# Performance work log

Hardware: AMD Instinct MI355X
Metric: run time of the kernel (lower is better)

The kernel has to match this reference:

```python
import jax, jax.numpy as jnp
import numpy as np

B, T, D, H, L = 32, 512, 1024, 1024, 2


def setup_inputs() -> dict:
    key = jax.random.key(0)
    ks = jax.random.split(key, 7)
    s_in = 1.0 / np.sqrt(D)
    s_h = 1.0 / np.sqrt(H)
    return {
        "x": jax.random.normal(ks[0], (B, T, D), dtype=jnp.float32),
        # layer 0: input_size = D
        "W_ih0": jax.random.uniform(ks[1], (4 * H, D), jnp.float32, -s_in, s_in),
        "b0": jax.random.uniform(ks[2], (4 * H,), jnp.float32, -s_in, s_in),
        "W_hh0": jax.random.uniform(ks[3], (4 * H, H), jnp.float32, -s_h, s_h),
        # layer 1: input_size = H
        "W_ih1": jax.random.uniform(ks[4], (4 * H, H), jnp.float32, -s_h, s_h),
        "b1": jax.random.uniform(ks[5], (4 * H,), jnp.float32, -s_h, s_h),
        "W_hh1": jax.random.uniform(ks[6], (4 * H, H), jnp.float32, -s_h, s_h),
    }


def _lstm_layer(x_seq, W_ih, b, W_hh):
    # x_seq: [T, B, Din]. Precompute the input-to-gate GEMM for all steps
    # (mathematically identical to per-step, but one big GEMM).
    gx = jnp.einsum('tbd,gd->tbg', x_seq, W_ih) + b  # [T, B, 4H]
    h0 = jnp.zeros((x_seq.shape[1], W_hh.shape[1]), x_seq.dtype)
    c0 = jnp.zeros_like(h0)

    def step(carry, gx_t):
        h, c = carry
        gates = gx_t + h @ W_hh.T  # [B, 4H]
        i, f, g, o = jnp.split(gates, 4, axis=-1)  # torch chunk order: i,f,g,o
        i = jax.nn.sigmoid(i)
        f = jax.nn.sigmoid(f)
        g = jnp.tanh(g)
        o = jax.nn.sigmoid(o)
        c_new = f * c + i * g
        h_new = o * jnp.tanh(c_new)
        return (h_new, c_new), h_new

    (h_n, c_n), hs = jax.lax.scan(step, (h0, c0), gx)
    return hs, h_n, c_n  # hs: [T, B, H]


def reference(x, W_ih0, b0, W_hh0, W_ih1, b1, W_hh1):
    xs = jnp.transpose(x, (1, 0, 2))  # batch_first -> [T, B, D]
    hs0, h0_n, c0_n = _lstm_layer(xs, W_ih0, b0, W_hh0)
    hs1, h1_n, c1_n = _lstm_layer(hs0, W_ih1, b1, W_hh1)
    output = jnp.transpose(hs1, (1, 0, 2))  # [B, T, H]
    h_n = jnp.stack([h0_n, h1_n], axis=0)  # [L, B, H]
    c_n = jnp.stack([c0_n, c1_n], axis=0)
    return output, (h_n, c_n)
```

## Files before the change

### kernel.cpp

```cpp
#include <hip/hip_runtime.h>
#include <stdint.h>

typedef __attribute__((ext_vector_type(8))) short short8;
typedef __attribute__((ext_vector_type(4))) short short4v;
typedef __attribute__((ext_vector_type(4))) float f32x4;
typedef __attribute__((ext_vector_type(4))) unsigned int u32x4;
typedef __attribute__((ext_vector_type(4))) int i32x4;
typedef __attribute__((ext_vector_type(2))) unsigned long long u64x2;

__device__ inline unsigned short f2bf(float f) {
  unsigned int u = __builtin_bit_cast(unsigned int, f);
  u += 0x7fffu + ((u >> 16) & 1u);
  return (unsigned short)(u >> 16);
}
__device__ inline float bf2f(unsigned short s) {
  return __builtin_bit_cast(float, (unsigned int)s << 16);
}

__device__ inline unsigned long long stale64(unsigned long long v) {
  unsigned long long x = v ^ 0x7f7f7f7f7f7f7f7full;
  return (x - 0x0001000100010001ull) & ~x & 0x8000800080008000ull;
}


__global__ __launch_bounds__(256) void cvt_x_kernel(const float* __restrict__ x,
                                                    short* __restrict__ xbf) {
  const int total = (16384 * 1024) / 4;
  for (int i = blockIdx.x * blockDim.x + threadIdx.x; i < total;
       i += gridDim.x * blockDim.x) {
    int d4 = i & 255;
    int m  = i >> 8;
    int t = m >> 5, b = m & 31;
    float4 v = *(const float4*)(x + ((size_t)b * 512 + t) * 1024 + (size_t)d4 * 4);
    short4v o;
    o.x = (short)f2bf(v.x); o.y = (short)f2bf(v.y);
    o.z = (short)f2bf(v.z); o.w = (short)f2bf(v.w);
    *(short4v*)(xbf + (size_t)m * 1024 + d4 * 4) = o;
  }
}

__global__ __launch_bounds__(256) void cvt_w_kernel(const float* __restrict__ W,
                                                    short* __restrict__ Wp) {
  const int total = (4096 * 1024) / 4;
  for (int i = blockIdx.x * blockDim.x + threadIdx.x; i < total;
       i += gridDim.x * blockDim.x) {
    int k4 = i & 255;
    int n  = i >> 8;
    int g = n & 3, j = n >> 2;
    float4 v = *(const float4*)(W + ((size_t)g * 1024 + j) * 1024 + (size_t)k4 * 4);
    short4v o;
    o.x = (short)f2bf(v.x); o.y = (short)f2bf(v.y);
    o.z = (short)f2bf(v.z); o.w = (short)f2bf(v.w);
    *(short4v*)(Wp + (size_t)n * 1024 + k4 * 4) = o;
  }
}

__global__ __launch_bounds__(256) void cvt_b_kernel(const float* __restrict__ b,
                                                    float* __restrict__ bp) {
  int n = blockIdx.x * blockDim.x + threadIdx.x;
  if (n < 4096) bp[n] = b[(n & 3) * 1024 + (n >> 2)];
}

__global__ __launch_bounds__(256) void gemm_bt(const short* __restrict__ A,
                                               const short* __restrict__ Bm,
                                               short* __restrict__ C) {
  const int n0 = blockIdx.x * 128;
  const int m0 = blockIdx.y * 128;
  const int tid = threadIdx.x;
  const int lane = tid & 63, wid = tid >> 6;
  const int wr = wid >> 1, wc = wid & 1;
  const int fr = lane & 15, fq = lane >> 4;

  __shared__ __align__(16) short As[128 * 32];
  __shared__ __align__(16) short Bs[128 * 32];

  f32x4 acc[4][4];
#pragma unroll
  for (int i = 0; i < 4; i++)
#pragma unroll
    for (int j = 0; j < 4; j++) acc[i][j] = (f32x4){0.f, 0.f, 0.f, 0.f};

  for (int kt = 0; kt < 1024; kt += 32) {
#pragma unroll
    for (int s = 0; s < 2; s++) {
      int c = tid + s * 256;
      int row = c >> 2;
      int off = (c & 3) * 8;
      *(u32x4*)&As[row * 32 + off] =
          *(const u32x4*)(A + (size_t)(n0 + row) * 1024 + kt + off);
      *(u32x4*)&Bs[row * 32 + off] =
          *(const u32x4*)(Bm + (size_t)(m0 + row) * 1024 + kt + off);
    }
    __syncthreads();
    short8 af[4], bf[4];
#pragma unroll
    for (int i = 0; i < 4; i++)
      af[i] = *(const short8*)&As[(wr * 64 + i * 16 + fr) * 32 + fq * 8];
#pragma unroll
    for (int j = 0; j < 4; j++)
      bf[j] = *(const short8*)&Bs[(wc * 64 + j * 16 + fr) * 32 + fq * 8];
#pragma unroll
    for (int i = 0; i < 4; i++)
#pragma unroll
      for (int j = 0; j < 4; j++)
        acc[i][j] = __builtin_amdgcn_mfma_f32_16x16x32_bf16(af[i], bf[j], acc[i][j], 0, 0, 0);
    __syncthreads();
  }

#pragma unroll
  for (int i = 0; i < 4; i++) {
#pragma unroll
    for (int j = 0; j < 4; j++) {
      int nq = n0 + wr * 64 + i * 16 + fq * 4;
      int m = m0 + wc * 64 + j * 16 + fr;
      int t = m >> 5, b = m & 31;
      unsigned long long pk = 0;
#pragma unroll
      for (int r = 0; r < 4; r++)
        pk |= (unsigned long long)f2bf(acc[i][j][r]) << (16 * r);
      *(unsigned long long*)&C[(size_t)t * 131072 + (size_t)b * 4096 + nq] = pk;
    }
  }
}

#define POLL8(HBP)                                                            \
  do {                                                                        \
    i32x4 r0, r1, r2, r3, r4, r5, r6, r7;                                     \
    while (true) {                                                            \
      asm volatile(                                                           \
          "global_load_dwordx4 %0, %8, %16 sc0 sc1\n\t"                       \
          "global_load_dwordx4 %1, %9, %16 sc0 sc1\n\t"                       \
          "global_load_dwordx4 %2, %10, %16 sc0 sc1\n\t"                      \
          "global_load_dwordx4 %3, %11, %16 sc0 sc1\n\t"                      \
          "global_load_dwordx4 %4, %12, %16 sc0 sc1\n\t"                      \
          "global_load_dwordx4 %5, %13, %16 sc0 sc1\n\t"                      \
          "global_load_dwordx4 %6, %14, %16 sc0 sc1\n\t"                      \
          "global_load_dwordx4 %7, %15, %16 sc0 sc1\n\t"                      \
          "s_waitcnt vmcnt(0)"                                                \
          : "=&v"(r0), "=&v"(r1), "=&v"(r2), "=&v"(r3), "=&v"(r4),            \
            "=&v"(r5), "=&v"(r6), "=&v"(r7)                                   \
          : "v"(soff[0]), "v"(soff[1]), "v"(soff[2]), "v"(soff[3]),           \
            "v"(soff[4]), "v"(soff[5]), "v"(soff[6]), "v"(soff[7]),           \
            "s"(HBP)                                                          \
          : "memory");                                                        \
      u64x2 q0 = __builtin_bit_cast(u64x2, r0), q1 = __builtin_bit_cast(u64x2, r1); \
      u64x2 q2 = __builtin_bit_cast(u64x2, r2), q3 = __builtin_bit_cast(u64x2, r3); \
      u64x2 q4 = __builtin_bit_cast(u64x2, r4), q5 = __builtin_bit_cast(u64x2, r5); \
      u64x2 q6 = __builtin_bit_cast(u64x2, r6), q7 = __builtin_bit_cast(u64x2, r7); \
      unsigned long long bad =                                                \
          stale64(q0.x) | stale64(q0.y) | stale64(q1.x) | stale64(q1.y) |     \
          stale64(q2.x) | stale64(q2.y) | stale64(q3.x) | stale64(q3.y) |     \
          stale64(q4.x) | stale64(q4.y) | stale64(q5.x) | stale64(q5.y) |     \
          stale64(q6.x) | stale64(q6.y) | stale64(q7.x) | stale64(q7.y);      \
      if (!bad) break;                                                        \
    }                                                                         \
    *(i32x4*)&img[widx[0]] = r0;                                              \
    *(i32x4*)&img[widx[1]] = r1;                                              \
    *(i32x4*)&img[widx[2]] = r2;                                              \
    *(i32x4*)&img[widx[3]] = r3;                                              \
    *(i32x4*)&img[widx[4]] = r4;                                              \
    *(i32x4*)&img[widx[5]] = r5;                                              \
    *(i32x4*)&img[widx[6]] = r6;                                              \
    *(i32x4*)&img[widx[7]] = r7;                                              \
  } while (0)

__global__ __launch_bounds__(512, 1) void lstm_fused(
    const short* __restrict__ gx0, const short* __restrict__ whh0,
    const float* __restrict__ b0p, const short* __restrict__ wih1,
    const short* __restrict__ whh1, const float* __restrict__ b1p,
    short* __restrict__ hs0, short* __restrict__ hs1,
    float* __restrict__ out, float* __restrict__ hn, float* __restrict__ cn) {
  const int tid = threadIdx.x;
  const int lane = tid & 63, w = tid >> 6;
  const int fr = lane & 15, fq = lane >> 4;

  __shared__ __align__(16) short img[32 * 1024];
  __shared__ __align__(16) float red[4 * 64 * 4];

  if (blockIdx.x < 64) {
    const int rg = (int)blockIdx.x >> 1, bg = (int)blockIdx.x & 1;
    const int n_base = rg * 128 + w * 16;
    const int b = bg * 16 + fr;
    const int jb = rg * 32 + w * 4;
    const int j = jb + fq;
    const int sw = fr & 7;

    const short* arow = whh0 + (size_t)(n_base + fr) * 1024 + fq * 8;
    short8 wreg[32];
#pragma unroll
    for (int kk = 0; kk < 32; kk++) wreg[kk] = *(const short8*)(arow + kk * 32);

    float bia[4];
#pragma unroll
    for (int r = 0; r < 4; r++) bia[r] = b0p[n_base + fq * 4 + r];

    unsigned int soff[4];
    int widx[4];
#pragma unroll
    for (int i = 0; i < 4; i++) {
      int ch = tid + i * 512;
      soff[i] = (unsigned int)ch * 16;
      int bb = ch >> 7, cc = ch & 127;
      widx[i] = bb * 1024 + ((cc ^ (bb & 7)) << 3);
    }

    float cell = 0.f;
    for (int t = 0; t < 512; ++t) {
      unsigned long long gq = *(const unsigned long long*)(
          gx0 + (size_t)t * 131072 + (size_t)b * 4096 + n_base + fq * 4);

      if (t > 0) {
        const short* hbp = hs0 + (size_t)(t - 1) * 32768 + bg * 16384;
        i32x4 r0, r1, r2, r3;
        while (true) {
          asm volatile(
              "global_load_dwordx4 %0, %4, %8 sc0 sc1\n\t"
              "global_load_dwordx4 %1, %5, %8 sc0 sc1\n\t"
              "global_load_dwordx4 %2, %6, %8 sc0 sc1\n\t"
              "global_load_dwordx4 %3, %7, %8 sc0 sc1\n\t"
              "s_waitcnt vmcnt(0)"
              : "=&v"(r0), "=&v"(r1), "=&v"(r2), "=&v"(r3)
              : "v"(soff[0]), "v"(soff[1]), "v"(soff[2]), "v"(soff[3]),
                "s"(hbp)
              : "memory");
          u64x2 q0 = __builtin_bit_cast(u64x2, r0);
          u64x2 q1 = __builtin_bit_cast(u64x2, r1);
          u64x2 q2 = __builtin_bit_cast(u64x2, r2);
          u64x2 q3 = __builtin_bit_cast(u64x2, r3);
          unsigned long long bad =
              stale64(q0.x) | stale64(q0.y) | stale64(q1.x) | stale64(q1.y) |
              stale64(q2.x) | stale64(q2.y) | stale64(q3.x) | stale64(q3.y);
          if (!bad) break;
        }
        *(i32x4*)&img[widx[0]] = r0;
        *(i32x4*)&img[widx[1]] = r1;
        *(i32x4*)&img[widx[2]] = r2;
        *(i32x4*)&img[widx[3]] = r3;
      }
      __syncthreads();

      f32x4 a0 = (f32x4){0.f,0.f,0.f,0.f}, a1 = (f32x4){0.f,0.f,0.f,0.f};
      f32x4 a2 = (f32x4){0.f,0.f,0.f,0.f}, a3 = (f32x4){0.f,0.f,0.f,0.f};
      if (t > 0) {
#pragma unroll
        for (int m = 0; m < 8; m++) {
          const int chb = fq + m * 16;
          short8 bv0 = *(const short8*)&img[fr * 1024 + (((chb + 0) ^ sw) << 3)];
          short8 bv1 = *(const short8*)&img[fr * 1024 + (((chb + 4) ^ sw) << 3)];
          short8 bv2 = *(const short8*)&img[fr * 1024 + (((chb + 8) ^ sw) << 3)];
          short8 bv3 = *(const short8*)&img[fr * 1024 + (((chb + 12) ^ sw) << 3)];
          a0 = __builtin_amdgcn_mfma_f32_16x16x32_bf16(wreg[4 * m + 0], bv0, a0, 0, 0, 0);
          a1 = __builtin_amdgcn_mfma_f32_16x16x32_bf16(wreg[4 * m + 1], bv1, a1, 0, 0, 0);
          a2 = __builtin_amdgcn_mfma_f32_16x16x32_bf16(wreg[4 * m + 2], bv2, a2, 0, 0, 0);
          a3 = __builtin_amdgcn_mfma_f32_16x16x32_bf16(wreg[4 * m + 3], bv3, a3, 0, 0, 0);
        }
      }

      float pre0 = (a0[0] + a1[0]) + (a2[0] + a3[0]) + bf2f((unsigned short)(gq & 0xFFFF)) + bia[0];
      float pre1 = (a0[1] + a1[1]) + (a2[1] + a3[1]) + bf2f((unsigned short)((gq >> 16) & 0xFFFF)) + bia[1];
      float pre2 = (a0[2] + a1[2]) + (a2[2] + a3[2]) + bf2f((unsigned short)((gq >> 32) & 0xFFFF)) + bia[2];
      float pre3 = (a0[3] + a1[3]) + (a2[3] + a3[3]) + bf2f((unsigned short)((gq >> 48) & 0xFFFF)) + bia[3];

      float iv = 1.f / (1.f + __expf(-pre0));
      float fv = 1.f / (1.f + __expf(-pre1));
      float gv = 2.f / (1.f + __expf(-2.f * pre2)) - 1.f;
      float ov = 1.f / (1.f + __expf(-pre3));
      cell = fv * cell + iv * gv;
      float h = ov * (2.f / (1.f + __expf(-2.f * cell)) - 1.f);

      unsigned int hu = (unsigned int)f2bf(h);
      unsigned int v1 = __shfl(hu, fr + 16);
      unsigned int v2 = __shfl(hu, fr + 32);
      unsigned int v3 = __shfl(hu, fr + 48);
      if (fq == 0) {
        unsigned long long pk = (unsigned long long)hu |
                                ((unsigned long long)v1 << 16) |
                                ((unsigned long long)v2 << 32) |
                                ((unsigned long long)v3 << 48);
        __hip_atomic_store(
            (unsigned long long*)(hs0 + (size_t)t * 32768 + (size_t)b * 1024 + jb),
            pk, __ATOMIC_RELAXED, __HIP_MEMORY_SCOPE_AGENT);
      }
      if (t == 511) {
        hn[b * 1024 + j] = h;
        cn[b * 1024 + j] = cell;
        break;
      }
      __syncthreads();
    }
  } else {
    const int idx = (int)blockIdx.x - 64;
    const int rg = idx >> 1, bg = idx & 1;
    const int wn = w & 3, mw = w >> 2;
    const int n_base = rg * 64 + wn * 16;
    const int b = bg * 16 + fr;
    const int jb = rg * 16 + wn * 4;
    const int j = jb + fq;
    const int sw = fr & 7;
    const int ib = mw << 14;

    const short* wsrc = mw ? wih1 : whh1;
    const short* arow = wsrc + (size_t)(n_base + fr) * 1024 + fq * 8;
    short8 wreg[32];
#pragma unroll
    for (int kk = 0; kk < 32; kk++) wreg[kk] = *(const short8*)(arow + kk * 32);

    float bia[4];
#pragma unroll
    for (int r = 0; r < 4; r++) bia[r] = b1p[n_base + fq * 4 + r];

    const int lt = tid & 255;
    unsigned int soff[8];
    int widx[8];
#pragma unroll
    for (int i = 0; i < 8; i++) {
      int ch = lt + i * 256;
      soff[i] = (unsigned int)ch * 16;
      int bb = ch >> 7, cc = ch & 127;
      widx[i] = ib + bb * 1024 + ((cc ^ (bb & 7)) << 3);
    }

    float cell = 0.f;
    for (int t = 0; t < 512; ++t) {
      if (mw) {
        const short* hbp = hs0 + (size_t)t * 32768 + bg * 16384;
        POLL8(hbp);
      } else if (t > 0) {
        const short* hbp = hs1 + (size_t)(t - 1) * 32768 + bg * 16384;
        POLL8(hbp);
      }
      __syncthreads();

      f32x4 a0 = (f32x4){0.f,0.f,0.f,0.f}, a1 = (f32x4){0.f,0.f,0.f,0.f};
      f32x4 a2 = (f32x4){0.f,0.f,0.f,0.f}, a3 = (f32x4){0.f,0.f,0.f,0.f};
      if (mw || t > 0) {
#pragma unroll
        for (int m = 0; m < 8; m++) {
          const int chb = fq + m * 16;
          short8 bv0 = *(const short8*)&img[ib + fr * 1024 + (((chb + 0) ^ sw) << 3)];
          short8 bv1 = *(const short8*)&img[ib + fr * 1024 + (((chb + 4) ^ sw) << 3)];
          short8 bv2 = *(const short8*)&img[ib + fr * 1024 + (((chb + 8) ^ sw) << 3)];
          short8 bv3 = *(const short8*)&img[ib + fr * 1024 + (((chb + 12) ^ sw) << 3)];
          a0 = __builtin_amdgcn_mfma_f32_16x16x32_bf16(wreg[4 * m + 0], bv0, a0, 0, 0, 0);
          a1 = __builtin_amdgcn_mfma_f32_16x16x32_bf16(wreg[4 * m + 1], bv1, a1, 0, 0, 0);
          a2 = __builtin_amdgcn_mfma_f32_16x16x32_bf16(wreg[4 * m + 2], bv2, a2, 0, 0, 0);
          a3 = __builtin_amdgcn_mfma_f32_16x16x32_bf16(wreg[4 * m + 3], bv3, a3, 0, 0, 0);
        }
      }
      f32x4 s4 = (a0 + a1) + (a2 + a3);
      if (mw) *(f32x4*)&red[(wn * 64 + lane) * 4] = s4;
      __syncthreads();

      if (!mw) {
        const f32x4 o4 = *(const f32x4*)&red[(wn * 64 + lane) * 4];
        float pre0 = s4[0] + o4[0] + bia[0];
        float pre1 = s4[1] + o4[1] + bia[1];
        float pre2 = s4[2] + o4[2] + bia[2];
        float pre3 = s4[3] + o4[3] + bia[3];

        float iv = 1.f / (1.f + __expf(-pre0));
        float fv = 1.f / (1.f + __expf(-pre1));
        float gv = 2.f / (1.f + __expf(-2.f * pre2)) - 1.f;
        float ov = 1.f / (1.f + __expf(-pre3));
        cell = fv * cell + iv * gv;
        float h = ov * (2.f / (1.f + __expf(-2.f * cell)) - 1.f);

        unsigned int hu = (unsigned int)f2bf(h);
        unsigned int v1 = __shfl(hu, fr + 16);
        unsigned int v2 = __shfl(hu, fr + 32);
        unsigned int v3 = __shfl(hu, fr + 48);
        if (fq == 0) {
          unsigned long long pk = (unsigned long long)hu |
                                  ((unsigned long long)v1 << 16) |
                                  ((unsigned long long)v2 << 32) |
                                  ((unsigned long long)v3 << 48);
          __hip_atomic_store(
              (unsigned long long*)(hs1 + (size_t)t * 32768 + (size_t)b * 1024 + jb),
              pk, __ATOMIC_RELAXED, __HIP_MEMORY_SCOPE_AGENT);
        }
        out[(size_t)b * 524288 + (size_t)t * 1024 + j] = h;
        if (t == 511) {
          hn[32768 + b * 1024 + j] = h;
          cn[32768 + b * 1024 + j] = cell;
        }
      }
      if (t == 511) break;
      __syncthreads();
    }
  }
}

extern "C" void kernel_launch(void* const* d_in, const int* in_sizes, int n_in,
                              void* d_out, int out_size, void* d_ws, size_t ws_size,
                              hipStream_t stream) {
  const float* x    = (const float*)d_in[0];
  const float* Wih0 = (const float*)d_in[1];
  const float* b0   = (const float*)d_in[2];
  const float* Whh0 = (const float*)d_in[3];
  const float* Wih1 = (const float*)d_in[4];
  const float* b1   = (const float*)d_in[5];
  const float* Whh1 = (const float*)d_in[6];

  float* out = (float*)d_out;
  float* hn  = out + 16777216;
  float* cn  = hn + 65536;

  char* ws = (char*)d_ws;
  size_t off = 0;
  auto carve = [&](size_t bytes) {
    char* p = ws + off;
    off += (bytes + 255) & ~(size_t)255;
    return p;
  };
  short* xbf   = (short*)carve(16384ull * 1024 * 2);
  short* wih0p = (short*)carve(4096ull * 1024 * 2);
  short* whh0p = (short*)carve(4096ull * 1024 * 2);
  short* wih1p = (short*)carve(4096ull * 1024 * 2);
  short* whh1p = (short*)carve(4096ull * 1024 * 2);
  float* b0p   = (float*)carve(4096 * 4);
  float* b1p   = (float*)carve(4096 * 4);
  short* gx    = (short*)carve(512ull * 4096 * 32 * 2);
  short* hs0   = (short*)carve(16384ull * 1024 * 2);

  hipLaunchKernelGGL(cvt_x_kernel, dim3(4096), dim3(256), 0, stream, x, xbf);
  hipLaunchKernelGGL(cvt_w_kernel, dim3(1024), dim3(256), 0, stream, Wih0, wih0p);
  hipLaunchKernelGGL(cvt_w_kernel, dim3(1024), dim3(256), 0, stream, Whh0, whh0p);
  hipLaunchKernelGGL(cvt_w_kernel, dim3(1024), dim3(256), 0, stream, Wih1, wih1p);
  hipLaunchKernelGGL(cvt_w_kernel, dim3(1024), dim3(256), 0, stream, Whh1, whh1p);
  hipLaunchKernelGGL(cvt_b_kernel, dim3(16), dim3(256), 0, stream, b0, b0p);
  hipLaunchKernelGGL(cvt_b_kernel, dim3(16), dim3(256), 0, stream, b1, b1p);
  hipMemsetAsync(hs0, 0x7F, 16384ull * 1024 * 2, stream);

  hipLaunchKernelGGL(gemm_bt, dim3(32, 128), dim3(256), 0, stream, wih0p, xbf, gx);

  short* hs1 = xbf;
  hipMemsetAsync(hs1, 0x7F, 16384ull * 1024 * 2, stream);

  hipLaunchKernelGGL(lstm_fused, dim3(192), dim3(512), 0, stream,
                     (const short*)gx, (const short*)whh0p, (const float*)b0p,
                     (const short*)wih1p, (const short*)whh1p, (const float*)b1p,
                     hs0, hs1, out, hn, cn);
}
```

Measured before the change: 2.119 ms.

## Fuse input-projection GEMM into persistent LSTM kernel with per-timestep readiness polling

Removes the separate x conversion and gemm_bt launches. Adds 64 producer blocks to the persistent LSTM kernel that compute the layer-0 input projection tile by tile, converting x from fp32 to bf16 on the fly, and publish results to gx with system-coherent stores. The layer-0 recurrence blocks poll gx for each timestep using a stale-sentinel check, so the GEMM overlaps with the serial recurrence instead of running before it. The cost is an extra memset of gx, 64 more blocks competing for CUs, and a dependence on tile order matching timestep order: tiles are processed in increasing m, which is the time-major order the consumers need.

New measurement: 2.917 ms. 37.6% more time.

```diff
diff --git a/kernel.cpp b/kernel.cpp
--- a/kernel.cpp
+++ b/kernel.cpp
@@ -22,22 +22,6 @@
   return (x - 0x0001000100010001ull) & ~x & 0x8000800080008000ull;
 }
 
-
-__global__ __launch_bounds__(256) void cvt_x_kernel(const float* __restrict__ x,
-                                                    short* __restrict__ xbf) {
-  const int total = (16384 * 1024) / 4;
-  for (int i = blockIdx.x * blockDim.x + threadIdx.x; i < total;
-       i += gridDim.x * blockDim.x) {
-    int d4 = i & 255;
-    int m  = i >> 8;
-    int t = m >> 5, b = m & 31;
-    float4 v = *(const float4*)(x + ((size_t)b * 512 + t) * 1024 + (size_t)d4 * 4);
-    short4v o;
-    o.x = (short)f2bf(v.x); o.y = (short)f2bf(v.y);
-    o.z = (short)f2bf(v.z); o.w = (short)f2bf(v.w);
-    *(short4v*)(xbf + (size_t)m * 1024 + d4 * 4) = o;
-  }
-}
 
 __global__ __launch_bounds__(256) void cvt_w_kernel(const float* __restrict__ W,
                                                     short* __restrict__ Wp) {
@@ -61,69 +45,7 @@
   if (n < 4096) bp[n] = b[(n & 3) * 1024 + (n >> 2)];
 }
 
-__global__ __launch_bounds__(256) void gemm_bt(const short* __restrict__ A,
-                                               const short* __restrict__ Bm,
-                                               short* __restrict__ C) {
-  const int n0 = blockIdx.x * 128;
-  const int m0 = blockIdx.y * 128;
-  const int tid = threadIdx.x;
-  const int lane = tid & 63, wid = tid >> 6;
-  const int wr = wid >> 1, wc = wid & 1;
-  const int fr = lane & 15, fq = lane >> 4;
-
-  __shared__ __align__(16) short As[128 * 32];
-  __shared__ __align__(16) short Bs[128 * 32];
-
-  f32x4 acc[4][4];
-#pragma unroll
-  for (int i = 0; i < 4; i++)
-#pragma unroll
-    for (int j = 0; j < 4; j++) acc[i][j] = (f32x4){0.f, 0.f, 0.f, 0.f};
-
-  for (int kt = 0; kt < 1024; kt += 32) {
-#pragma unroll
-    for (int s = 0; s < 2; s++) {
-      int c = tid + s * 256;
-      int row = c >> 2;
-      int off = (c & 3) * 8;
-      *(u32x4*)&As[row * 32 + off] =
-          *(const u32x4*)(A + (size_t)(n0 + row) * 1024 + kt + off);
-      *(u32x4*)&Bs[row * 32 + off] =
-          *(const u32x4*)(Bm + (size_t)(m0 + row) * 1024 + kt + off);
-    }
-    __syncthreads();
-    short8 af[4], bf[4];
-#pragma unroll
-    for (int i = 0; i < 4; i++)
-      af[i] = *(const short8*)&As[(wr * 64 + i * 16 + fr) * 32 + fq * 8];
-#pragma unroll
-    for (int j = 0; j < 4; j++)
-      bf[j] = *(const short8*)&Bs[(wc * 64 + j * 16 + fr) * 32 + fq * 8];
-#pragma unroll
-    for (int i = 0; i < 4; i++)
-#pragma unroll
-      for (int j = 0; j < 4; j++)
-        acc[i][j] = __builtin_amdgcn_mfma_f32_16x16x32_bf16(af[i], bf[j], acc[i][j], 0, 0, 0);
-    __syncthreads();
-  }
-
-#pragma unroll
-  for (int i = 0; i < 4; i++) {
-#pragma unroll
-    for (int j = 0; j < 4; j++) {
-      int nq = n0 + wr * 64 + i * 16 + fq * 4;
-      int m = m0 + wc * 64 + j * 16 + fr;
-      int t = m >> 5, b = m & 31;
-      unsigned long long pk = 0;
-#pragma unroll
-      for (int r = 0; r < 4; r++)
-        pk |= (unsigned long long)f2bf(acc[i][j][r]) << (16 * r);
-      *(unsigned long long*)&C[(size_t)t * 131072 + (size_t)b * 4096 + nq] = pk;
-    }
-  }
-}
-
-#define POLL8(HBP)                                                            \
+#define PULL8_SPIN(HBP)                                                       \
   do {                                                                        \
     i32x4 r0, r1, r2, r3, r4, r5, r6, r7;                                     \
     while (true) {                                                            \
@@ -165,9 +87,10 @@
   } while (0)
 
 __global__ __launch_bounds__(512, 1) void lstm_fused(
-    const short* __restrict__ gx0, const short* __restrict__ whh0,
-    const float* __restrict__ b0p, const short* __restrict__ wih1,
-    const short* __restrict__ whh1, const float* __restrict__ b1p,
+    const float* __restrict__ x, const short* __restrict__ wih0p,
+    const short* __restrict__ whh0, const float* __restrict__ b0p,
+    const short* __restrict__ wih1, const short* __restrict__ whh1,
+    const float* __restrict__ b1p, short* __restrict__ gx0,
     short* __restrict__ hs0, short* __restrict__ hs1,
     float* __restrict__ out, float* __restrict__ hn, float* __restrict__ cn) {
   const int tid = threadIdx.x;
@@ -178,10 +101,79 @@
   __shared__ __align__(16) float red[4 * 64 * 4];
 
   if (blockIdx.x < 64) {
-    const int rg = (int)blockIdx.x >> 1, bg = (int)blockIdx.x & 1;
-    const int n_base = rg * 128 + w * 16;
+    short* As = img;
+    short* Bs = img + 4096;
+    const int wr = w >> 1, wc = w & 1;
+
+    for (int T = (int)blockIdx.x; T < 4096; T += 64) {
+      const int mt = T >> 5, nt = T & 31;
+      const int n0 = nt * 128, m0 = mt * 128;
+
+      f32x4 acc[2][4];
+#pragma unroll
+      for (int i = 0; i < 2; i++)
+#pragma unroll
+        for (int j = 0; j < 4; j++) acc[i][j] = (f32x4){0.f, 0.f, 0.f, 0.f};
+
+      for (int kt = 0; kt < 1024; kt += 32) {
+        {
+          int row = tid >> 2;
+          int off = (tid & 3) * 8;
+          *(u32x4*)&As[row * 32 + off] =
+              *(const u32x4*)(wih0p + (size_t)(n0 + row) * 1024 + kt + off);
+          int m = m0 + row;
+          int tt = m >> 5, bb = m & 31;
+          const float* xp = x + ((size_t)bb * 512 + tt) * 1024 + kt + off;
+          float4 va = *(const float4*)xp;
+          float4 vb = *(const float4*)(xp + 4);
+          short8 o;
+          o[0] = (short)f2bf(va.x); o[1] = (short)f2bf(va.y);
+          o[2] = (short)f2bf(va.z); o[3] = (short)f2bf(va.w);
+          o[4] = (short)f2bf(vb.x); o[5] = (short)f2bf(vb.y);
+          o[6] = (short)f2bf(vb.z); o[7] = (short)f2bf(vb.w);
+          *(short8*)&Bs[row * 32 + off] = o;
+        }
+        __syncthreads();
+        short8 af[2], bfr[4];
+#pragma unroll
+        for (int i = 0; i < 2; i++)
+          af[i] = *(const short8*)&As[(wr * 32 + i * 16 + fr) * 32 + fq * 8];
+#pragma unroll
+        for (int j = 0; j < 4; j++)
+          bfr[j] = *(const short8*)&Bs[(wc * 64 + j * 16 + fr) * 32 + fq * 8];
+#pragma unroll
+        for (int i = 0; i < 2; i++)
+#pragma unroll
+          for (int j = 0; j < 4; j++)
+            acc[i][j] = __builtin_amdgcn_mfma_f32_16x16x32_bf16(af[i], bfr[j], acc[i][j], 0, 0, 0);
+        __syncthreads();
+      }
+
+#pragma unroll
+      for (int i = 0; i < 2; i++) {
+#pragma unroll
+        for (int j = 0; j < 4; j++) {
+          int nq = n0 + wr * 32 + i * 16 + fq * 4;
+          int m = m0 + wc * 64 + j * 16 + fr;
+          int tt = m >> 5, bb = m & 31;
+          unsigned long long pk = 0;
+#pragma unroll
+          for (int r = 0; r < 4; r++)
+            pk |= (unsigned long long)f2bf(acc[i][j][r]) << (16 * r);
+          unsigned int voff =
+              (unsigned int)(((unsigned)tt * 131072u + (unsigned)bb * 4096u +
+                              (unsigned)nq) * 2u);
+          asm volatile("global_store_dwordx2 %0, %1, %2 sc0 sc1"
+                       :: "v"(voff), "v"(pk), "s"(gx0) : "memory");
+        }
+      }
+    }
+  } else if (blockIdx.x < 128) {
+    const int idx0 = (int)blockIdx.x - 64;
+    const int bg = idx0 & 1;
+    const int n_base = (idx0 >> 1) * 128 + w * 16;
     const int b = bg * 16 + fr;
-    const int jb = rg * 32 + w * 4;
+    const int jb = (idx0 >> 1) * 32 + w * 4;
     const int j = jb + fq;
     const int sw = fr & 7;
 
@@ -203,11 +195,21 @@
       int bb = ch >> 7, cc = ch & 127;
       widx[i] = bb * 1024 + ((cc ^ (bb & 7)) << 3);
     }
+    const unsigned int goff = (unsigned int)(((unsigned)b * 4096 + n_base + fq * 4) * 2);
 
     float cell = 0.f;
     for (int t = 0; t < 512; ++t) {
-      unsigned long long gq = *(const unsigned long long*)(
-          gx0 + (size_t)t * 131072 + (size_t)b * 4096 + n_base + fq * 4);
+      unsigned long long gq;
+      {
+        const short* gb = gx0 + (size_t)t * 131072;
+        while (true) {
+          asm volatile("global_load_dwordx2 %0, %1, %2 sc0 sc1\n\t"
+                       "s_waitcnt vmcnt(0)"
+                       : "=v"(gq) : "v"(goff), "s"(gb) : "memory");
+          if (!__any((int)(stale64(gq) != 0ull))) break;
+          __builtin_amdgcn_s_sleep(1);
+        }
+      }
 
       if (t > 0) {
         const short* hbp = hs0 + (size_t)(t - 1) * 32768 + bg * 16384;
@@ -289,7 +291,7 @@
       __syncthreads();
     }
   } else {
-    const int idx = (int)blockIdx.x - 64;
+    const int idx = (int)blockIdx.x - 128;
     const int rg = idx >> 1, bg = idx & 1;
     const int wn = w & 3, mw = w >> 2;
     const int n_base = rg * 64 + wn * 16;
@@ -324,10 +326,10 @@
     for (int t = 0; t < 512; ++t) {
       if (mw) {
         const short* hbp = hs0 + (size_t)t * 32768 + bg * 16384;
-        POLL8(hbp);
+        PULL8_SPIN(hbp);
       } else if (t > 0) {
         const short* hbp = hs1 + (size_t)(t - 1) * 32768 + bg * 16384;
-        POLL8(hbp);
+        PULL8_SPIN(hbp);
       }
       __syncthreads();
 
@@ -412,7 +414,6 @@
     off += (bytes + 255) & ~(size_t)255;
     return p;
   };
-  short* xbf   = (short*)carve(16384ull * 1024 * 2);
   short* wih0p = (short*)carve(4096ull * 1024 * 2);
   short* whh0p = (short*)carve(4096ull * 1024 * 2);
   short* wih1p = (short*)carve(4096ull * 1024 * 2);
@@ -421,23 +422,20 @@
   float* b1p   = (float*)carve(4096 * 4);
   short* gx    = (short*)carve(512ull * 4096 * 32 * 2);
   short* hs0   = (short*)carve(16384ull * 1024 * 2);
-
-  hipLaunchKernelGGL(cvt_x_kernel, dim3(4096), dim3(256), 0, stream, x, xbf);
+  short* hs1   = (short*)carve(16384ull * 1024 * 2);
+
   hipLaunchKernelGGL(cvt_w_kernel, dim3(1024), dim3(256), 0, stream, Wih0, wih0p);
   hipLaunchKernelGGL(cvt_w_kernel, dim3(1024), dim3(256), 0, stream, Whh0, whh0p);
   hipLaunchKernelGGL(cvt_w_kernel, dim3(1024), dim3(256), 0, stream, Wih1, wih1p);
   hipLaunchKernelGGL(cvt_w_kernel, dim3(1024), dim3(256), 0, stream, Whh1, whh1p);
   hipLaunchKernelGGL(cvt_b_kernel, dim3(16), dim3(256), 0, stream, b0, b0p);
   hipLaunchKernelGGL(cvt_b_kernel, dim3(16), dim3(256), 0, stream, b1, b1p);
-  hipMemsetAsync(hs0, 0x7F, 16384ull * 1024 * 2, stream);
-
-  hipLaunchKernelGGL(gemm_bt, dim3(32, 128), dim3(256), 0, stream, wih0p, xbf, gx);
-
-  short* hs1 = xbf;
-  hipMemsetAsync(hs1, 0x7F, 16384ull * 1024 * 2, stream);
-
-  hipLaunchKernelGGL(lstm_fused, dim3(192), dim3(512), 0, stream,
-                     (const short*)gx, (const short*)whh0p, (const float*)b0p,
+  (void)hipMemsetAsync(gx,  0x7F, 512ull * 4096 * 32 * 2, stream);
+  (void)hipMemsetAsync(hs0, 0x7F, 16384ull * 1024 * 2, stream);
+  (void)hipMemsetAsync(hs1, 0x7F, 16384ull * 1024 * 2, stream);
+
+  hipLaunchKernelGGL(lstm_fused, dim3(256), dim3(512), 0, stream,
+                     x, (const short*)wih0p, (const short*)whh0p, (const float*)b0p,
                      (const short*)wih1p, (const short*)whh1p, (const float*)b1p,
-                     hs0, hs1, out, hn, cn);
-}
+                     gx, hs0, hs1, out, hn, cn);
+}
```
